# Kernel optimization log

Measured on AMD Instinct MI355X. Metric: run time of the kernel, lower is better.

The kernel has to match this reference:

```python
import jax, jax.numpy as jnp
import numpy as np

T, B, D, H = 1024, 8, 1024, 16
NH = D // H  # 64, per-head width (nhid)
W_SCALE = 0.02


def setup_inputs() -> dict:
    key = jax.random.key(0)
    ks = jax.random.split(key, 10)
    return {
        "input_tensor": jax.random.normal(ks[0], (T, B, D), jnp.float32),
        "keys_vector": jax.random.normal(ks[1], (T, B, D), jnp.float32),
        "values_vector": jax.random.normal(ks[2], (T, B, D), jnp.float32),
        # per-head projection weights: [H, D, NH]
        "Wq": jax.random.normal(ks[3], (H, D, NH), jnp.float32) * W_SCALE,
        "bq": jnp.zeros((H, NH), jnp.float32),
        "Wk": jax.random.normal(ks[4], (H, D, NH), jnp.float32) * W_SCALE,
        "bk": jnp.zeros((H, NH), jnp.float32),
        "Wv": jax.random.normal(ks[5], (H, D, NH), jnp.float32) * W_SCALE,
        "bv": jnp.zeros((H, NH), jnp.float32),
        # output projection after concatenating heads
        "Wo": jax.random.normal(ks[6], (D, D), jnp.float32) * W_SCALE,
        "bo": jnp.zeros((D,), jnp.float32),
        "mask": 1,  # True: causal (growing key slice per timestep)
    }


def reference(input_tensor, keys_vector, values_vector, Wq, bq, Wk, bk, Wv, bv, Wo, bo, mask):
    # Vectorized equivalent of the per-timestep loop: query at step t attends
    # to keys/values[:t+1] when mask is set, else to the full sequence.
    q = jnp.einsum('tbd,hdk->tbhk', input_tensor, Wq) + bq   # [T,B,H,NH]
    k = jnp.einsum('sbd,hdk->sbhk', keys_vector, Wk) + bk    # [T,B,H,NH]
    v = jnp.einsum('sbd,hdk->sbhk', values_vector, Wv) + bv  # [T,B,H,NH]

    scale = 1.0 / jnp.sqrt(jnp.float32(NH))
    scores = jnp.einsum('tbhk,sbhk->bhts', q, k) * scale     # [B,H,T,T]
    if mask:
        causal = jnp.tril(jnp.ones((T, T), dtype=bool))      # s <= t
        scores = jnp.where(causal[None, None], scores, jnp.float32(-1e9))
    attn = jax.nn.softmax(scores, axis=-1)                   # over key dim s

    out = jnp.einsum('bhts,sbhk->tbhk', attn, v)             # [T,B,H,NH]
    out = out.reshape(T, B, D)                               # concat heads
    return out @ Wo.T + bo                                   # [T,B,D]
```

## Files before the change

### kernel.cpp

```cpp
#include <hip/hip_runtime.h>

typedef short bf16x8 __attribute__((ext_vector_type(8)));
typedef float f32x4 __attribute__((ext_vector_type(4)));
typedef float f32x16 __attribute__((ext_vector_type(16)));

typedef const __attribute__((address_space(1))) void* gptr_t;
typedef __attribute__((address_space(3))) void* sptr_t;

#define Z16 {0.f,0.f,0.f,0.f,0.f,0.f,0.f,0.f,0.f,0.f,0.f,0.f,0.f,0.f,0.f,0.f}

__device__ __forceinline__ void glds16(const void* g, void* s) {
  __builtin_amdgcn_global_load_lds((gptr_t)g, (sptr_t)s, 16, 0, 0);
}

__device__ __forceinline__ unsigned short f2bf(float x) {
  unsigned u = __float_as_uint(x);
  u = u + 0x7fffu + ((u >> 16) & 1u);
  return (unsigned short)(u >> 16);
}

__device__ __forceinline__ unsigned packbf(float lo, float hi) {
  return (unsigned)f2bf(lo) | (((unsigned)f2bf(hi)) << 16);
}

__global__ void cvtall(const float* __restrict__ X, const float* __restrict__ KY,
                       const float* __restrict__ VY, const float* __restrict__ Wo,
                       unsigned short* __restrict__ XB, unsigned short* __restrict__ WOB) {
  int stride = gridDim.x * blockDim.x;
  for (int i = blockIdx.x * blockDim.x + threadIdx.x; i < 6553600; i += stride) {
    const float* in; unsigned short* out; int k;
    if (i < 2097152)      { in = X;  out = XB;            k = i; }
    else if (i < 4194304) { in = KY; out = XB + 8388608;  k = i - 2097152; }
    else if (i < 6291456) { in = VY; out = XB + 16777216; k = i - 4194304; }
    else                  { in = Wo; out = WOB;           k = i - 6291456; }
    float4 v = ((const float4*)in)[k];
    uint2 r;
    r.x = packbf(v.x, v.y);
    r.y = packbf(v.z, v.w);
    ((uint2*)out)[k] = r;
  }
}

__global__ __launch_bounds__(256) void wtrans(const float* __restrict__ Wq,
                                              const float* __restrict__ Wk,
                                              const float* __restrict__ Wv,
                                              unsigned short* __restrict__ WT) {
  int m = blockIdx.y >> 4, h = blockIdx.y & 15, d0 = blockIdx.x * 64;
  const float* src = (m == 0 ? Wq : (m == 1 ? Wk : Wv)) + (size_t)h * 65536;
  __shared__ float tile[64][65];
  int c = (threadIdx.x & 15) * 4, r0 = threadIdx.x >> 4;
#pragma unroll
  for (int rr = 0; rr < 4; ++rr) {
    int dr = rr * 16 + r0;
    float4 v = *(const float4*)(src + (size_t)(d0 + dr) * 64 + c);
    tile[dr][c + 0] = v.x; tile[dr][c + 1] = v.y;
    tile[dr][c + 2] = v.z; tile[dr][c + 3] = v.w;
  }
  __syncthreads();
#pragma unroll
  for (int rr = 0; rr < 4; ++rr) {
    int kr = rr * 16 + r0;
    uint2 pk;
    pk.x = packbf(tile[c + 0][kr], tile[c + 1][kr]);
    pk.y = packbf(tile[c + 2][kr], tile[c + 3][kr]);
    *(uint2*)(WT + ((size_t)(m * 1024 + h * 64 + kr)) * 1024 + d0 + c) = pk;
  }
}

template <int MODE>
__global__ __launch_bounds__(256) void gemm_k(const unsigned short* __restrict__ Ab,
                                              const unsigned short* __restrict__ Bb,
                                              const float* __restrict__ bi0,
                                              const float* __restrict__ bi1,
                                              const float* __restrict__ bi2,
                                              void* __restrict__ outp) {
  const int K = 1024;
  int z = blockIdx.z;
  const unsigned short* A = Ab + (size_t)z * 8192 * 1024;
  const unsigned short* BT = Bb + (size_t)z * 1024 * 1024;
  const float* bias = (MODE == 0) ? (z == 0 ? bi0 : (z == 1 ? bi1 : bi2)) : bi0;
  int m0 = blockIdx.x * 128, n0 = blockIdx.y * 128;
  __shared__ __align__(16) char lds[32768];
  char* As = lds;
  char* Bs = lds + 16384;
  int tid = threadIdx.x, w = tid >> 6, l = tid & 63, ml = l & 15, hi = l >> 4;
  int wr = (w >> 1) * 64, wc = (w & 1) * 64;
  int srow = l >> 3;
  int kphys = (l & 7) << 4;
  f32x4 acc[4][4] = {};
  for (int kt = 0; kt < K; kt += 64) {
    __syncthreads();
#pragma unroll
    for (int i = 0; i < 4; ++i) {
      int c = w * 4 + i;
      int row = c * 8 + srow;
      int klog = kphys ^ ((row & 7) << 4);
      glds16((const char*)(A + (size_t)(m0 + row) * K + kt) + klog, As + c * 1024);
      glds16((const char*)(BT + (size_t)(n0 + row) * K + kt) + klog, Bs + c * 1024);
    }
    __syncthreads();
#pragma unroll
    for (int ks = 0; ks < 2; ++ks) {
      bf16x8 af[4], bfr[4];
#pragma unroll
      for (int mi = 0; mi < 4; ++mi) {
        int row = wr + mi * 16 + ml;
        af[mi] = *(const bf16x8*)(As + row * 128 + ((ks * 64 + (hi << 4)) ^ ((row & 7) << 4)));
      }
#pragma unroll
      for (int ni = 0; ni < 4; ++ni) {
        int row = wc + ni * 16 + ml;
        bfr[ni] = *(const bf16x8*)(Bs + row * 128 + ((ks * 64 + (hi << 4)) ^ ((row & 7) << 4)));
      }
#pragma unroll
      for (int mi = 0; mi < 4; ++mi)
#pragma unroll
        for (int ni = 0; ni < 4; ++ni)
          acc[mi][ni] = __builtin_amdgcn_mfma_f32_16x16x32_bf16(af[mi], bfr[ni], acc[mi][ni], 0, 0, 0);
    }
  }
  if (MODE == 1) {
#pragma unroll
    for (int mi = 0; mi < 4; ++mi) {
#pragma unroll
      for (int ni = 0; ni < 4; ++ni) {
        int col = n0 + wc + ni * 16 + ml;
        float bv = bias[col];
#pragma unroll
        for (int r = 0; r < 4; ++r) {
          int row = m0 + wr + mi * 16 + (hi << 2) + r;
          ((float*)outp)[(size_t)row * 1024 + col] = acc[mi][ni][r] + bv;
        }
      }
    }
    return;
  }
  __syncthreads();
#pragma unroll
  for (int mi = 0; mi < 4; ++mi) {
#pragma unroll
    for (int ni = 0; ni < 4; ++ni) {
      int col = wc + ni * 16 + ml;
      float bv = bias[n0 + col];
#pragma unroll
      for (int r = 0; r < 4; ++r) {
        int row = wr + mi * 16 + (hi << 2) + r;
        float v = acc[mi][ni][r] + bv;
        float pv = __shfl_xor(v, 1);
        unsigned pk = (ml & 1) ? packbf(pv, v) : packbf(v, pv);
        *(unsigned*)(lds + row * 256 + (((col * 2) & ~3) ^ ((row & 7) << 4))) = pk;
      }
    }
  }
  __syncthreads();
  unsigned short* ob = (unsigned short*)outp + (size_t)z * 8388608;
  if (z != 2) {
    int rr = tid >> 1, hh = tid & 1;
    int t = (m0 + rr) >> 3, b = (m0 + rr) & 7;
    int hg = (n0 >> 6) + hh;
    unsigned short* dst = ob + (size_t)(b * 16 + hg) * 65536 + (size_t)t * 64;
#pragma unroll
    for (int j = 0; j < 8; ++j) {
      uint4 d = *(uint4*)(lds + rr * 256 + ((hh * 128 + j * 16) ^ ((rr & 7) << 4)));
      *(uint4*)(dst + j * 8) = d;
    }
  } else {
    int t0 = m0 >> 3;
#pragma unroll
    for (int q = 0; q < 4; ++q) {
      int run = q * 256 + tid;
      int k = run & 63;
      int bh2 = run >> 6;
      int b = bh2 >> 1, hh = bh2 & 1;
      int colb = (hh * 64 + k) * 2;
      union { unsigned short u[16]; uint4 v[2]; } tmp;
#pragma unroll
      for (int tp = 0; tp < 16; ++tp) {
        int rowt = tp * 8 + b;
        tmp.u[tp] = *(unsigned short*)(lds + rowt * 256 + (colb ^ ((b & 7) << 4)));
      }
      int hg = (n0 >> 6) + hh;
      unsigned short* dst = ob + (size_t)(b * 16 + hg) * 65536 + (size_t)k * 1024 + t0;
      *(uint4*)dst = tmp.v[0];
      *(uint4*)(dst + 8) = tmp.v[1];
    }
  }
}

__global__ __launch_bounds__(512, 4) void attn_k(const unsigned short* __restrict__ Qp,
                                                 const unsigned short* __restrict__ Kp,
                                                 const unsigned short* __restrict__ VTp,
                                                 unsigned short* __restrict__ Op,
                                                 const int* __restrict__ maskp) {
  int lin = blockIdx.x;
  int xcd = lin & 7, idx = lin >> 3;
  int bh = xcd + 8 * (idx >> 2);
  int j = idx & 3;
  const size_t base = (size_t)bh * 65536;
  int tid = threadIdx.x, w = tid >> 6, l = tid & 63;
  int ml5 = l & 31, hi1 = l >> 5;
  int half = w & 1, pi = w >> 1;
  int stripe = (pi == 0) ? j : (pi == 1) ? (15 - j) : (pi == 2) ? (7 - j) : (8 + j);
  int tw0 = stripe * 64 + half * 32;
  int t_glob = tw0 + ml5;
  __shared__ __align__(16) char lds[32768];
  int msk = *maskp;
  const float CE = 0.18033688011112042f;
  bf16x8 bq[4];
#pragma unroll
  for (int kd = 0; kd < 4; ++kd)
    bq[kd] = *(const bf16x8*)(Qp + base + (size_t)t_glob * 64 + kd * 16 + hi1 * 8);
  f32x16 o0 = Z16, o1 = Z16;
  float m_run = -3e38f, l_run = 0.f;
  int nt = msk ? (16 - j) : 16;
  int diag = stripe;
  int srow = l >> 3, kphys = (l & 7) << 4;
  int row = w * 8 + srow;
  int klog = kphys ^ (srow << 4);
  int swz = (ml5 & 7) << 4;
  glds16((const char*)(Kp + base + (size_t)row * 64) + klog, lds + w * 1024);
  glds16((const char*)(VTp + base + (size_t)row * 1024) + klog, lds + 8192 + w * 1024);
  __syncthreads();
  int cur = 0;
  for (int st = 0; st < nt; ++st) {
    if (st + 1 < nt) {
      char* nb = lds + (cur ^ 1) * 16384;
      glds16((const char*)(Kp + base + (size_t)((st + 1) * 64 + row) * 64) + klog, nb + w * 1024);
      glds16((const char*)(VTp + base + (size_t)row * 1024 + (st + 1) * 64) + klog, nb + 8192 + w * 1024);
    }
    if (!msk || st <= diag) {
      char* Ks = lds + cur * 16384;
      char* Vs = Ks + 8192;
      f32x16 s0 = Z16, s1 = Z16;
      __builtin_amdgcn_s_setprio(1);
#pragma unroll
      for (int kd = 0; kd < 4; ++kd) {
        int koff = kd * 32 + hi1 * 16;
        bf16x8 a0 = *(const bf16x8*)(Ks + ml5 * 128 + (koff ^ swz));
        bf16x8 a1 = *(const bf16x8*)(Ks + (32 + ml5) * 128 + (koff ^ swz));
        s0 = __builtin_amdgcn_mfma_f32_32x32x16_bf16(a0, bq[kd], s0, 0, 0, 0);
        s1 = __builtin_amdgcn_mfma_f32_32x32x16_bf16(a1, bq[kd], s1, 0, 0, 0);
      }
      __builtin_amdgcn_s_setprio(0);
      if (msk && st == diag) {
#pragma unroll
        for (int r = 0; r < 16; ++r) {
          int sl = st * 64 + (r & 3) + 8 * (r >> 2) + 4 * hi1;
          if (sl > t_glob) s0[r] = -1e30f;
          if (sl + 32 > t_glob) s1[r] = -1e30f;
        }
      }
      float t8[8];
#pragma unroll
      for (int r = 0; r < 8; ++r)
        t8[r] = fmaxf(fmaxf(s0[r], s0[r + 8]), fmaxf(s1[r], s1[r + 8]));
      float tm = fmaxf(fmaxf(fmaxf(t8[0], t8[1]), fmaxf(t8[2], t8[3])),
                       fmaxf(fmaxf(t8[4], t8[5]), fmaxf(t8[6], t8[7])));
      tm = fmaxf(tm, __shfl_xor(tm, 32));
      float m_old = m_run;
      float m_new = fmaxf(m_old, tm);
      m_run = m_new;
      float sc2 = exp2f((m_old - m_new) * CE);
      float mC = m_new * CE;
#pragma unroll
      for (int r = 0; r < 16; ++r) {
        s0[r] = exp2f(fmaf(s0[r], CE, -mC));
        s1[r] = exp2f(fmaf(s1[r], CE, -mC));
      }
      float a8[8];
#pragma unroll
      for (int r = 0; r < 8; ++r)
        a8[r] = (s0[r] + s0[r + 8]) + (s1[r] + s1[r + 8]);
      float ps = ((a8[0] + a8[1]) + (a8[2] + a8[3])) + ((a8[4] + a8[5]) + (a8[6] + a8[7]));
      ps += __shfl_xor(ps, 32);
      l_run = l_run * sc2 + ps;
#pragma unroll
      for (int r = 0; r < 16; ++r) { o0[r] *= sc2; o1[r] *= sc2; }
      unsigned cc0[4][2], cc1[4][2];
#pragma unroll
      for (int q = 0; q < 4; ++q) {
        cc0[q][0] = packbf(s0[4 * q + 0], s0[4 * q + 1]);
        cc0[q][1] = packbf(s0[4 * q + 2], s0[4 * q + 3]);
        cc1[q][0] = packbf(s1[4 * q + 0], s1[4 * q + 1]);
        cc1[q][1] = packbf(s1[4 * q + 2], s1[4 * q + 3]);
      }
#define CCa(a, p) ((a) < 4 ? cc0[(a) & 3][p] : cc1[(a) & 3][p])
      union U4 { unsigned u[4]; bf16x8 v; };
      bf16x8 pb[4];
#pragma unroll
      for (int kb = 0; kb < 4; ++kb) {
        U4 t;
#pragma unroll
        for (int p = 0; p < 2; ++p) {
          unsigned x = CCa(2 * kb, p), y = CCa(2 * kb + 1, p);
          unsigned v = hi1 ? x : y;
          unsigned wv = hi1 ? y : x;
          unsigned vs = __shfl_xor(v, 32);
          t.u[p]     = hi1 ? vs : wv;
          t.u[2 + p] = hi1 ? wv : vs;
        }
        pb[kb] = t.v;
      }
#undef CCa
      __builtin_amdgcn_s_setprio(1);
#pragma unroll
      for (int kb = 0; kb < 4; ++kb) {
        int koff = kb * 32 + hi1 * 16;
        bf16x8 v0 = *(const bf16x8*)(Vs + ml5 * 128 + (koff ^ swz));
        bf16x8 v1 = *(const bf16x8*)(Vs + (32 + ml5) * 128 + (koff ^ swz));
        o0 = __builtin_amdgcn_mfma_f32_32x32x16_bf16(v0, pb[kb], o0, 0, 0, 0);
        o1 = __builtin_amdgcn_mfma_f32_32x32x16_bf16(v1, pb[kb], o1, 0, 0, 0);
      }
      __builtin_amdgcn_s_setprio(0);
    }
    __syncthreads();
    cur ^= 1;
  }
  float rl = 1.0f / l_run;
  int b = bh >> 4, h = bh & 15;
  unsigned short* orow = Op + (size_t)(t_glob * 8 + b) * 1024 + h * 64;
#pragma unroll
  for (int q2 = 0; q2 < 4; ++q2) {
    uint2 pk0, pk1;
    pk0.x = packbf(o0[4 * q2 + 0] * rl, o0[4 * q2 + 1] * rl);
    pk0.y = packbf(o0[4 * q2 + 2] * rl, o0[4 * q2 + 3] * rl);
    *(uint2*)(orow + 4 * hi1 + 8 * q2) = pk0;
    pk1.x = packbf(o1[4 * q2 + 0] * rl, o1[4 * q2 + 1] * rl);
    pk1.y = packbf(o1[4 * q2 + 2] * rl, o1[4 * q2 + 3] * rl);
    *(uint2*)(orow + 32 + 4 * hi1 + 8 * q2) = pk1;
  }
}

extern "C" void kernel_launch(void* const* d_in, const int* in_sizes, int n_in,
                              void* d_out, int out_size, void* d_ws, size_t ws_size,
                              hipStream_t stream) {
  const float* X  = (const float*)d_in[0];
  const float* KY = (const float*)d_in[1];
  const float* VY = (const float*)d_in[2];
  const float* Wq = (const float*)d_in[3];
  const float* bq = (const float*)d_in[4];
  const float* Wk = (const float*)d_in[5];
  const float* bk = (const float*)d_in[6];
  const float* Wv = (const float*)d_in[7];
  const float* bv = (const float*)d_in[8];
  const float* Wo = (const float*)d_in[9];
  const float* bo = (const float*)d_in[10];
  const int* mask = (const int*)d_in[11];
  char* ws = (char*)d_ws;
  unsigned short* XB  = (unsigned short*)(ws);
  unsigned short* WT  = (unsigned short*)(ws + 48ll * 1024 * 1024);
  unsigned short* WOB = (unsigned short*)(ws + 54ll * 1024 * 1024);
  unsigned short* QP  = (unsigned short*)(ws + 56ll * 1024 * 1024);
  unsigned short* OP  = (unsigned short*)(ws + 104ll * 1024 * 1024);

  cvtall<<<2048, 256, 0, stream>>>(X, KY, VY, Wo, XB, WOB);
  wtrans<<<dim3(16, 48), 256, 0, stream>>>(Wq, Wk, Wv, WT);
  gemm_k<0><<<dim3(64, 8, 3), 256, 0, stream>>>(XB, WT, bq, bk, bv, QP);
  attn_k<<<512, 512, 0, stream>>>(QP, QP + 8388608, QP + 16777216, OP, mask);
  gemm_k<1><<<dim3(64, 8, 1), 256, 0, stream>>>(OP, WOB, bo, bo, bo, d_out);
}
```

Measured before the change: 199.4 us.

## Double-buffer GEMM LDS tiles and stage fp32 output through LDS

The projection GEMM now prefetches the next K tile into a second LDS buffer while computing on the current one, with one barrier per iteration instead of two. MFMA sections run at raised wave priority. The fp32 output epilogue writes through swizzled LDS so global stores become row-contiguous 16-byte writes. LDS use doubles to 64KB, which may reduce blocks per CU.

Result: no change. 202.5 us (+1.5%).

```diff
diff --git a/kernel.cpp b/kernel.cpp
--- a/kernel.cpp
+++ b/kernel.cpp
@@ -80,25 +80,38 @@
   const unsigned short* BT = Bb + (size_t)z * 1024 * 1024;
   const float* bias = (MODE == 0) ? (z == 0 ? bi0 : (z == 1 ? bi1 : bi2)) : bi0;
   int m0 = blockIdx.x * 128, n0 = blockIdx.y * 128;
-  __shared__ __align__(16) char lds[32768];
-  char* As = lds;
-  char* Bs = lds + 16384;
+  __shared__ __align__(16) char lds[65536];
   int tid = threadIdx.x, w = tid >> 6, l = tid & 63, ml = l & 15, hi = l >> 4;
   int wr = (w >> 1) * 64, wc = (w & 1) * 64;
   int srow = l >> 3;
   int kphys = (l & 7) << 4;
   f32x4 acc[4][4] = {};
-  for (int kt = 0; kt < K; kt += 64) {
-    __syncthreads();
-#pragma unroll
-    for (int i = 0; i < 4; ++i) {
-      int c = w * 4 + i;
-      int row = c * 8 + srow;
-      int klog = kphys ^ ((row & 7) << 4);
-      glds16((const char*)(A + (size_t)(m0 + row) * K + kt) + klog, As + c * 1024);
-      glds16((const char*)(BT + (size_t)(n0 + row) * K + kt) + klog, Bs + c * 1024);
-    }
-    __syncthreads();
+  int stg_c = 0;
+#pragma unroll
+  for (int i = 0; i < 4; ++i) {
+    int c = w * 4 + i;
+    int row = c * 8 + srow;
+    int klog = kphys ^ ((row & 7) << 4);
+    glds16((const char*)(A + (size_t)(m0 + row) * K) + klog, lds + c * 1024);
+    glds16((const char*)(BT + (size_t)(n0 + row) * K) + klog, lds + 16384 + c * 1024);
+  }
+  __syncthreads();
+  int cur = 0;
+  for (int kt16 = 0; kt16 < 16; ++kt16) {
+    if (kt16 + 1 < 16) {
+      char* nb = lds + (cur ^ 1) * 32768;
+      int kt = (kt16 + 1) * 64;
+#pragma unroll
+      for (int i = 0; i < 4; ++i) {
+        int c = w * 4 + i;
+        int row = c * 8 + srow;
+        int klog = kphys ^ ((row & 7) << 4);
+        glds16((const char*)(A + (size_t)(m0 + row) * K + kt) + klog, nb + c * 1024);
+        glds16((const char*)(BT + (size_t)(n0 + row) * K + kt) + klog, nb + 16384 + c * 1024);
+      }
+    }
+    char* As = lds + cur * 32768;
+    char* Bs = As + 16384;
 #pragma unroll
     for (int ks = 0; ks < 2; ++ks) {
       bf16x8 af[4], bfr[4];
@@ -112,30 +125,43 @@
         int row = wc + ni * 16 + ml;
         bfr[ni] = *(const bf16x8*)(Bs + row * 128 + ((ks * 64 + (hi << 4)) ^ ((row & 7) << 4)));
       }
+      __builtin_amdgcn_s_setprio(1);
 #pragma unroll
       for (int mi = 0; mi < 4; ++mi)
 #pragma unroll
         for (int ni = 0; ni < 4; ++ni)
           acc[mi][ni] = __builtin_amdgcn_mfma_f32_16x16x32_bf16(af[mi], bfr[ni], acc[mi][ni], 0, 0, 0);
-    }
+      __builtin_amdgcn_s_setprio(0);
+    }
+    __syncthreads();
+    cur ^= 1;
   }
   if (MODE == 1) {
 #pragma unroll
     for (int mi = 0; mi < 4; ++mi) {
 #pragma unroll
       for (int ni = 0; ni < 4; ++ni) {
-        int col = n0 + wc + ni * 16 + ml;
-        float bv = bias[col];
+        int col = wc + ni * 16 + ml;
+        float bv = bias[n0 + col];
 #pragma unroll
         for (int r = 0; r < 4; ++r) {
-          int row = m0 + wr + mi * 16 + (hi << 2) + r;
-          ((float*)outp)[(size_t)row * 1024 + col] = acc[mi][ni][r] + bv;
+          int row = wr + mi * 16 + (hi << 2) + r;
+          int byte = col * 4;
+          *(float*)(lds + row * 512 + ((byte & ~15) ^ ((row & 7) << 4)) + (byte & 15)) =
+              acc[mi][ni][r] + bv;
         }
       }
     }
+    __syncthreads();
+    int rr = tid >> 1, hh = tid & 1;
+    float* drow = (float*)outp + (size_t)(m0 + rr) * 1024 + n0 + hh * 64;
+#pragma unroll
+    for (int jj = 0; jj < 16; ++jj) {
+      uint4 d = *(uint4*)(lds + rr * 512 + ((hh * 256 + jj * 16) ^ ((rr & 7) << 4)));
+      *(uint4*)(drow + jj * 4) = d;
+    }
     return;
   }
-  __syncthreads();
 #pragma unroll
   for (int mi = 0; mi < 4; ++mi) {
 #pragma unroll
```
